# Kernel optimization log

Hardware: AMD Instinct MI355X
Metric: run time of the kernel (lower is better)

Reference implementation:

```python
import jax, jax.numpy as jnp
import numpy as np

B, S, D, H, DI, L = 16, 80, 512, 64, 2048, 6  # batch, seq, d_model, d_lstm(=d_v), d_inner, n_layers
EPS = 1e-6


def _layer_norm(x, g, b):
    m = jnp.mean(x, axis=-1, keepdims=True)
    v = jnp.mean((x - m) ** 2, axis=-1, keepdims=True)
    return (x - m) * jax.lax.rsqrt(v + EPS) * g + b


def _lstm_last(gx, whh):
    # gx: [T, N, 4H] precomputed input-to-gate projections (bias=False LSTM)
    N = gx.shape[1]
    Hh = whh.shape[1]
    init = (jnp.zeros((N, Hh), gx.dtype), jnp.zeros((N, Hh), gx.dtype))

    def step(carry, g_in):
        h, c = carry
        gates = g_in + h @ whh.T  # [N, 4H], torch gate order i,f,g,o
        i, f, g, o = jnp.split(gates, 4, axis=-1)
        c = jax.nn.sigmoid(f) * c + jax.nn.sigmoid(i) * jnp.tanh(g)
        h = jax.nn.sigmoid(o) * jnp.tanh(c)
        return (h, c), None

    (h, _), _ = jax.lax.scan(step, init, gx)
    return h  # [N, H]


def _perm_indices():
    # deterministic janossy permutation: identity with position i swapped to last
    idx = np.arange(S)
    P = np.tile(idx, (S, 1))
    P[idx, idx] = S - 1
    P[idx, S - 1] = idx
    return jnp.asarray(P)  # [S, S]


def _janossy_layer(q, g, b, wih, whh, wfc, P):
    # q: [B, S, D]
    x = _layer_norm(q, g, b)
    # project inputs to gates once, then gather permutations of the projection
    xg = jnp.einsum('bsd,gd->sbg', x, wih)  # [S, B, 4H]
    pg = xg[P]  # [S_i, S_t, B, 4H]: for each output position i, the permuted sequence
    pg = pg.transpose(1, 0, 2, 3).reshape(S, S * B, 4 * H)  # time-major, fold i into batch
    h = _lstm_last(pg, whh)  # [S*B, H]
    h = h.reshape(S, B, H).transpose(1, 0, 2)  # [B, S, H]
    return h @ wfc.T + q  # fc (dropout=identity in eval) + residual


def _ffn(q, g, b, w1, b1, w2, b2):
    x = _layer_norm(q, g, b)
    return jax.nn.relu(x @ w1.T + b1) @ w2.T + b2 + q


def setup_inputs() -> dict:
    key = jax.random.key(0)
    ks = jax.random.split(key, 10)
    n = lambda k, s, sc: jax.random.normal(k, s, jnp.float32) * sc
    return {
        'src_seq': jax.random.normal(ks[0], (B, S, D), jnp.float32),
        'trg_seq': jax.random.normal(ks[1], (B, S, D), jnp.float32),
        'ln1_g': jnp.ones((L, D), jnp.float32),
        'ln1_b': jnp.zeros((L, D), jnp.float32),
        'wih': n(ks[2], (L, 4 * H, D), 0.04),
        'whh': n(ks[3], (L, 4 * H, H), 0.1),
        'wfc': n(ks[4], (L, D, H), 0.05),
        'ln2_g': jnp.ones((L, D), jnp.float32),
        'ln2_b': jnp.zeros((L, D), jnp.float32),
        'w1': n(ks[5], (L, DI, D), 0.03),
        'b1': jnp.zeros((L, DI), jnp.float32),
        'w2': n(ks[6], (L, D, DI), 0.02),
        'b2': jnp.zeros((L, D), jnp.float32),
        'lnf_g': jnp.ones((D,), jnp.float32),
        'lnf_b': jnp.zeros((D,), jnp.float32),
        'wprj': n(ks[7], (1, D), 0.05),
    }


def reference(src_seq, trg_seq, ln1_g, ln1_b, wih, whh, wfc, ln2_g, ln2_b,
              w1, b1, w2, b2, lnf_g, lnf_b, wprj):
    P = _perm_indices()
    x = src_seq
    for l in range(L):  # small fixed layer count
        x = _janossy_layer(x, ln1_g[l], ln1_b[l], wih[l], whh[l], wfc[l], P)
        x = _ffn(x, ln2_g[l], ln2_b[l], w1[l], b1[l], w2[l], b2[l])
    x = _layer_norm(x, lnf_g, lnf_b)
    seq_logit = x @ wprj.T  # [B, S, 1]
    return seq_logit
```

## Files before the change

kernel.cpp:

```cpp
#include <hip/hip_runtime.h>
#include <hip/hip_bf16.h>

#define B_ 16
#define S_ 80
#define D_ 512
#define H_ 64
#define DI_ 2048
#define L_ 6
#define G4H 256
#define NROW (B_ * S_)
#define EPS_ 1e-6f

typedef __attribute__((ext_vector_type(8))) short short8;
typedef __attribute__((ext_vector_type(4))) float f32x4;

__device__ __forceinline__ float sigmoidf_(float x) {
    return __fdividef(1.0f, 1.0f + __expf(-x));
}
__device__ __forceinline__ float tanh_(float x) {
    return __fdividef(2.0f, 1.0f + __expf(-2.0f * x)) - 1.0f;
}
__device__ __forceinline__ short f2bf(float f) {
    __hip_bfloat16 h = __float2bfloat16(f);
    return *reinterpret_cast<short*>(&h);
}

__device__ __forceinline__ void lds_barrier() {
    __asm__ volatile("s_waitcnt lgkmcnt(0)\n\ts_barrier" ::: "memory");
}

__global__ __launch_bounds__(256)
void w2bf_all_kernel(const float* __restrict__ s0, int n0, __hip_bfloat16* __restrict__ d0,
                     const float* __restrict__ s1, int n1, __hip_bfloat16* __restrict__ d1,
                     const float* __restrict__ s2, int n2, __hip_bfloat16* __restrict__ d2,
                     const float* __restrict__ s3, int n3, __hip_bfloat16* __restrict__ d3) {
    int i = blockIdx.x * 256 + threadIdx.x;
    const float* s; __hip_bfloat16* d;
    if (i < n0)      { s = s0; d = d0; }
    else if ((i -= n0) < n1) { s = s1; d = d1; }
    else if ((i -= n1) < n2) { s = s2; d = d2; }
    else if ((i -= n2) < n3) { s = s3; d = d3; }
    else return;
    float4 v = reinterpret_cast<const float4*>(s)[i];
    short4 o;
    o.x = f2bf(v.x); o.y = f2bf(v.y); o.z = f2bf(v.z); o.w = f2bf(v.w);
    reinterpret_cast<short4*>(d)[i] = o;
}

__global__ __launch_bounds__(256)
void ln_kernel(const float* __restrict__ x, const float* __restrict__ g,
               const float* __restrict__ b, __hip_bfloat16* __restrict__ out) {
    int row = blockIdx.x;
    int t = threadIdx.x;
    const float* xr = x + (size_t)row * D_;
    float v0 = xr[t], v1 = xr[t + 256];
    __shared__ float ws4[4], qs4[4];
    float s = v0 + v1;
    #pragma unroll
    for (int o = 32; o > 0; o >>= 1) s += __shfl_down(s, o);
    if ((t & 63) == 0) ws4[t >> 6] = s;
    __syncthreads();
    float m = (ws4[0] + ws4[1] + ws4[2] + ws4[3]) * (1.0f / (float)D_);
    float d0 = v0 - m, d1 = v1 - m;
    float q = d0 * d0 + d1 * d1;
    #pragma unroll
    for (int o = 32; o > 0; o >>= 1) q += __shfl_down(q, o);
    if ((t & 63) == 0) qs4[t >> 6] = q;
    __syncthreads();
    float rs = rsqrtf((qs4[0] + qs4[1] + qs4[2] + qs4[3]) * (1.0f / (float)D_) + EPS_);
    __hip_bfloat16* orow = out + (size_t)row * D_;
    orow[t]       = __float2bfloat16(d0 * rs * g[t]       + b[t]);
    orow[t + 256] = __float2bfloat16(d1 * rs * g[t + 256] + b[t + 256]);
}

template<int WITH_BIAS, int WITH_RELU, int WITH_RES, int OUT_MODE>
__global__ __launch_bounds__(256)
void mfma_gemm(const __hip_bfloat16* __restrict__ A, const __hip_bfloat16* __restrict__ W,
               const float* __restrict__ bias, const float* __restrict__ res,
               void* __restrict__ C, int M, int N, int K) {
    const int LDT = 72;
    __shared__ short As[64 * LDT];
    __shared__ short Ws[64 * LDT];

    int tid  = threadIdx.x;
    int wave = tid >> 6, lane = tid & 63;
    int quad = lane >> 4, l16 = lane & 15;
    int m_off = (wave >> 1) * 32, n_off = (wave & 1) * 32;
    int m0 = blockIdx.y * 64, n0 = blockIdx.x * 64;

    int r = tid >> 2, c = tid & 3;
    const short* Ag = reinterpret_cast<const short*>(A);
    const short* Wg = reinterpret_cast<const short*>(W);

    f32x4 acc00 = {0.f,0.f,0.f,0.f}, acc01 = acc00, acc10 = acc00, acc11 = acc00;

    short8 avA[2], avW[2];
    auto load_tile = [&](int k0) {
        const short* arow = &Ag[(size_t)(m0 + r) * K + k0 + c * 16];
        avA[0] = *reinterpret_cast<const short8*>(arow);
        avA[1] = *reinterpret_cast<const short8*>(arow + 8);
        const short* wrow = &Wg[(size_t)(n0 + r) * K + k0 + c * 16];
        avW[0] = *reinterpret_cast<const short8*>(wrow);
        avW[1] = *reinterpret_cast<const short8*>(wrow + 8);
    };

    load_tile(0);
    for (int k0 = 0; k0 < K; k0 += 64) {
        lds_barrier();
        *reinterpret_cast<short8*>(&As[r * LDT + c * 16])     = avA[0];
        *reinterpret_cast<short8*>(&As[r * LDT + c * 16 + 8]) = avA[1];
        *reinterpret_cast<short8*>(&Ws[r * LDT + c * 16])     = avW[0];
        *reinterpret_cast<short8*>(&Ws[r * LDT + c * 16 + 8]) = avW[1];
        lds_barrier();
        if (k0 + 64 < K) load_tile(k0 + 64);

        #pragma unroll
        for (int kc = 0; kc < 2; kc++) {
            short8 a0 = *reinterpret_cast<const short8*>(&As[(m_off + l16) * LDT + kc * 32 + quad * 8]);
            short8 a1 = *reinterpret_cast<const short8*>(&As[(m_off + 16 + l16) * LDT + kc * 32 + quad * 8]);
            short8 b0 = *reinterpret_cast<const short8*>(&Ws[(n_off + l16) * LDT + kc * 32 + quad * 8]);
            short8 b1 = *reinterpret_cast<const short8*>(&Ws[(n_off + 16 + l16) * LDT + kc * 32 + quad * 8]);
            acc00 = __builtin_amdgcn_mfma_f32_16x16x32_bf16(a0, b0, acc00, 0, 0, 0);
            acc01 = __builtin_amdgcn_mfma_f32_16x16x32_bf16(a0, b1, acc01, 0, 0, 0);
            acc10 = __builtin_amdgcn_mfma_f32_16x16x32_bf16(a1, b0, acc10, 0, 0, 0);
            acc11 = __builtin_amdgcn_mfma_f32_16x16x32_bf16(a1, b1, acc11, 0, 0, 0);
        }
    }

    f32x4 accs[2][2] = {{acc00, acc01}, {acc10, acc11}};
    #pragma unroll
    for (int fi = 0; fi < 2; fi++) {
        #pragma unroll
        for (int fj = 0; fj < 2; fj++) {
            int coln = n0 + n_off + fj * 16 + l16;
            float bv = WITH_BIAS ? bias[coln] : 0.0f;
            #pragma unroll
            for (int rr = 0; rr < 4; rr++) {
                int rowm = m0 + m_off + fi * 16 + quad * 4 + rr;
                float v = accs[fi][fj][rr];
                if (WITH_BIAS) v += bv;
                if (WITH_RELU) v = fmaxf(v, 0.0f);
                if (WITH_RES)  v += res[(size_t)rowm * N + coln];
                if (OUT_MODE == 0) {
                    reinterpret_cast<float*>(C)[(size_t)rowm * N + coln] = v;
                } else if (OUT_MODE == 1) {
                    reinterpret_cast<__hip_bfloat16*>(C)[(size_t)rowm * N + coln] = __float2bfloat16(v);
                } else {
                    int b_ = rowm / S_;
                    int s_ = rowm - b_ * S_;
                    int gate = coln >> 6, u = coln & 63;
                    int half = b_ >> 3, slot = b_ & 7;
                    reinterpret_cast<float*>(C)[
                        ((((size_t)(s_ * 2 + half) * 4 + gate) * 64 + u) << 3) + slot] = v;
                }
            }
        }
    }
}

__global__ __launch_bounds__(256)
void lstm_fc_kernel(const float* __restrict__ xg5,
                    const float* __restrict__ whh,
                    const __hip_bfloat16* __restrict__ wfcb,
                    const float* __restrict__ g2,
                    const float* __restrict__ b2v,
                    float* __restrict__ xcur,
                    __hip_bfloat16* __restrict__ lnb) {
    const int i    = blockIdx.x;
    const int bh   = blockIdx.y;
    const int tid  = threadIdx.x;
    const int wave = tid >> 6, lane = tid & 63;
    const int quad = lane >> 4, l16 = lane & 15;
    const int unit = wave * 16 + l16;

    short8 bfrag[4][2];
    #pragma unroll
    for (int g = 0; g < 4; g++) {
        const float* wr = &whh[(size_t)(g * 64 + unit) * H_];
        #pragma unroll
        for (int kc = 0; kc < 2; kc++) {
            float4 x0 = *(const float4*)(wr + kc * 32 + quad * 8);
            float4 x1 = *(const float4*)(wr + kc * 32 + quad * 8 + 4);
            short8 v;
            v[0] = f2bf(x0.x); v[1] = f2bf(x0.y); v[2] = f2bf(x0.z); v[3] = f2bf(x0.w);
            v[4] = f2bf(x1.x); v[5] = f2bf(x1.y); v[6] = f2bf(x1.z); v[7] = f2bf(x1.w);
            bfrag[g][kc] = v;
        }
    }

    __shared__ __attribute__((aligned(16))) short hsh[2][16][72];
    __shared__ float sred[4][4][2][2];
    for (int idx = tid; idx < 2 * 16 * 72; idx += 256)
        reinterpret_cast<short*>(hsh)[idx] = 0;

    float cst[2] = {0.f, 0.f};

    size_t xoff[4];
    #pragma unroll
    for (int g = 0; g < 4; g++)
        xoff[g] = ((((size_t)bh * 4 + g) * 64 + unit) << 3) + quad * 2;

    auto xload = [&](float2 (&xv)[4], int t) {
        int s = (t == i) ? (S_ - 1) : ((t == S_ - 1) ? i : t);
        const float* base = xg5 + (size_t)s * 4096;
        #pragma unroll
        for (int g = 0; g < 4; g++)
            xv[g] = *reinterpret_cast<const float2*>(base + xoff[g]);
    };

    float2 xvA[4], xvB[4];
    xload(xvA, 0);
    xload(xvB, 1);

    lds_barrier();

    const f32x4 zacc = {0.f, 0.f, 0.f, 0.f};

    auto stepv = [&](int t, float2 (&xc)[4]) {
        const int pb = t & 1;
        short8 af0 = *reinterpret_cast<const short8*>(&hsh[pb][l16][quad * 8]);
        short8 af1 = *reinterpret_cast<const short8*>(&hsh[pb][l16][32 + quad * 8]);

        f32x4 p0 = __builtin_amdgcn_mfma_f32_16x16x32_bf16(af0, bfrag[0][0], zacc, 0, 0, 0);
        f32x4 q0 = __builtin_amdgcn_mfma_f32_16x16x32_bf16(af1, bfrag[0][1], zacc, 0, 0, 0);
        f32x4 p1 = __builtin_amdgcn_mfma_f32_16x16x32_bf16(af0, bfrag[1][0], zacc, 0, 0, 0);
        f32x4 q1 = __builtin_amdgcn_mfma_f32_16x16x32_bf16(af1, bfrag[1][1], zacc, 0, 0, 0);
        f32x4 p2 = __builtin_amdgcn_mfma_f32_16x16x32_bf16(af0, bfrag[2][0], zacc, 0, 0, 0);
        f32x4 q2 = __builtin_amdgcn_mfma_f32_16x16x32_bf16(af1, bfrag[2][1], zacc, 0, 0, 0);
        f32x4 p3 = __builtin_amdgcn_mfma_f32_16x16x32_bf16(af0, bfrag[3][0], zacc, 0, 0, 0);
        f32x4 q3 = __builtin_amdgcn_mfma_f32_16x16x32_bf16(af1, bfrag[3][1], zacc, 0, 0, 0);

        float gi0 = p0[0] + q0[0] + xc[0].x, gi1 = p0[1] + q0[1] + xc[0].y;
        float gf0 = p1[0] + q1[0] + xc[1].x, gf1 = p1[1] + q1[1] + xc[1].y;
        float gg0 = p2[0] + q2[0] + xc[2].x, gg1 = p2[1] + q2[1] + xc[2].y;
        float go0 = p3[0] + q3[0] + xc[3].x, go1 = p3[1] + q3[1] + xc[3].y;

        if (t + 2 < S_) xload(xc, t + 2);

        {
            float ig = sigmoidf_(gi0);
            float fg = sigmoidf_(gf0);
            float gv = tanh_(gg0);
            float og = sigmoidf_(go0);
            float cc = fg * cst[0] + ig * gv;
            cst[0] = cc;
            hsh[pb ^ 1][quad * 4 + 0][unit] = f2bf(og * tanh_(cc));
        }
        {
            float ig = sigmoidf_(gi1);
            float fg = sigmoidf_(gf1);
            float gv = tanh_(gg1);
            float og = sigmoidf_(go1);
            float cc = fg * cst[1] + ig * gv;
            cst[1] = cc;
            hsh[pb ^ 1][quad * 4 + 1][unit] = f2bf(og * tanh_(cc));
        }
        lds_barrier();
    };

    for (int t = 0; t < S_; t += 2) { stepv(t, xvA); stepv(t + 1, xvB); }

    {
        const short* wf = reinterpret_cast<const short*>(wfcb);
        short8 af0 = *reinterpret_cast<const short8*>(&hsh[0][l16][quad * 8]);
        short8 af1 = *reinterpret_cast<const short8*>(&hsh[0][l16][32 + quad * 8]);

        f32x4 facc[8];
        #pragma unroll
        for (int nn = 0; nn < 8; nn++) {
            int col16 = (wave * 8 + nn) * 16 + l16;
            short8 w0 = *reinterpret_cast<const short8*>(&wf[(size_t)col16 * H_ + quad * 8]);
            short8 w1 = *reinterpret_cast<const short8*>(&wf[(size_t)col16 * H_ + 32 + quad * 8]);
            f32x4 a = __builtin_amdgcn_mfma_f32_16x16x32_bf16(af0, w0, zacc, 0, 0, 0);
            facc[nn] = __builtin_amdgcn_mfma_f32_16x16x32_bf16(af1, w1, a, 0, 0, 0);
        }

        float xn[8][2];
        float ssum[2] = {0.f, 0.f}, sq[2] = {0.f, 0.f};
        #pragma unroll
        for (int nn = 0; nn < 8; nn++) {
            int col = (wave * 8 + nn) * 16 + l16;
            #pragma unroll
            for (int rr = 0; rr < 2; rr++) {
                int b = bh * 8 + quad * 2 + rr;
                size_t adr = ((size_t)b * S_ + i) * D_ + col;
                float v = facc[nn][rr] + xcur[adr];
                xn[nn][rr] = v;
                xcur[adr] = v;
                ssum[rr] += v;
                sq[rr]   += v * v;
            }
        }
        #pragma unroll
        for (int m = 1; m < 16; m <<= 1) {
            ssum[0] += __shfl_xor(ssum[0], m); ssum[1] += __shfl_xor(ssum[1], m);
            sq[0]   += __shfl_xor(sq[0], m);   sq[1]   += __shfl_xor(sq[1], m);
        }
        if (l16 == 0) {
            #pragma unroll
            for (int rr = 0; rr < 2; rr++) {
                sred[wave][quad][rr][0] = ssum[rr];
                sred[wave][quad][rr][1] = sq[rr];
            }
        }
        lds_barrier();
        float mmean[2], rstd[2];
        #pragma unroll
        for (int rr = 0; rr < 2; rr++) {
            float s = sred[0][quad][rr][0] + sred[1][quad][rr][0]
                    + sred[2][quad][rr][0] + sred[3][quad][rr][0];
            float q = sred[0][quad][rr][1] + sred[1][quad][rr][1]
                    + sred[2][quad][rr][1] + sred[3][quad][rr][1];
            float m = s * (1.0f / (float)D_);
            mmean[rr] = m;
            rstd[rr]  = rsqrtf(q * (1.0f / (float)D_) - m * m + EPS_);
        }
        #pragma unroll
        for (int nn = 0; nn < 8; nn++) {
            int col = (wave * 8 + nn) * 16 + l16;
            float gv = g2[col], bv = b2v[col];
            #pragma unroll
            for (int rr = 0; rr < 2; rr++) {
                int b = bh * 8 + quad * 2 + rr;
                lnb[((size_t)b * S_ + i) * D_ + col] =
                    __float2bfloat16((xn[nn][rr] - mmean[rr]) * rstd[rr] * gv + bv);
            }
        }
    }
}

__global__ __launch_bounds__(256)
void final_kernel(const float* __restrict__ x, const float* __restrict__ g,
                  const float* __restrict__ b, const float* __restrict__ wprj,
                  float* __restrict__ out) {
    int row = blockIdx.x;
    int t = threadIdx.x;
    const float* xr = x + (size_t)row * D_;
    float v0 = xr[t], v1 = xr[t + 256];
    __shared__ float red[256];
    red[t] = v0 + v1;
    __syncthreads();
    for (int o = 128; o > 0; o >>= 1) { if (t < o) red[t] += red[t + o]; __syncthreads(); }
    float m = red[0] * (1.0f / (float)D_);
    __syncthreads();
    float d0 = v0 - m, d1 = v1 - m;
    red[t] = d0 * d0 + d1 * d1;
    __syncthreads();
    for (int o = 128; o > 0; o >>= 1) { if (t < o) red[t] += red[t + o]; __syncthreads(); }
    float rs = rsqrtf(red[0] * (1.0f / (float)D_) + EPS_);
    __syncthreads();
    float y0 = (d0 * rs * g[t] + b[t]) * wprj[t];
    float y1 = (d1 * rs * g[t + 256] + b[t + 256]) * wprj[t + 256];
    red[t] = y0 + y1;
    __syncthreads();
    for (int o = 128; o > 0; o >>= 1) { if (t < o) red[t] += red[t + o]; __syncthreads(); }
    if (t == 0) out[row] = red[0];
}

extern "C" void kernel_launch(void* const* d_in, const int* in_sizes, int n_in,
                              void* d_out, int out_size, void* d_ws, size_t ws_size,
                              hipStream_t stream) {
    const float* src   = (const float*)d_in[0];
    const float* ln1_g = (const float*)d_in[2];
    const float* ln1_b = (const float*)d_in[3];
    const float* wih   = (const float*)d_in[4];
    const float* whh   = (const float*)d_in[5];
    const float* wfc   = (const float*)d_in[6];
    const float* ln2_g = (const float*)d_in[7];
    const float* ln2_b = (const float*)d_in[8];
    const float* w1    = (const float*)d_in[9];
    const float* b1    = (const float*)d_in[10];
    const float* w2    = (const float*)d_in[11];
    const float* b2    = (const float*)d_in[12];
    const float* lnf_g = (const float*)d_in[13];
    const float* lnf_b = (const float*)d_in[14];
    const float* wprj  = (const float*)d_in[15];
    float* out = (float*)d_out;

    char* ws = (char*)d_ws;
    float* xcur = (float*)ws;                       ws += (size_t)NROW * D_  * 4;
    __hip_bfloat16* lnb = (__hip_bfloat16*)ws;      ws += (size_t)NROW * D_  * 2;
    float* xg5  = (float*)ws;                       ws += (size_t)S_ * 4096  * 4;
    __hip_bfloat16* f1  = (__hip_bfloat16*)ws;      ws += (size_t)NROW * DI_ * 2;
    __hip_bfloat16* wihb = (__hip_bfloat16*)ws;     ws += (size_t)L_ * G4H * D_ * 2;
    __hip_bfloat16* wfcb = (__hip_bfloat16*)ws;     ws += (size_t)L_ * D_ * H_ * 2;
    __hip_bfloat16* w1b  = (__hip_bfloat16*)ws;     ws += (size_t)L_ * DI_ * D_ * 2;
    __hip_bfloat16* w2b  = (__hip_bfloat16*)ws;     ws += (size_t)L_ * D_ * DI_ * 2;

    {
        int n0 = L_ * G4H * D_ / 4;
        int n1 = L_ * D_ * H_ / 4;
        int n2 = L_ * DI_ * D_ / 4;
        int n3 = L_ * D_ * DI_ / 4;
        int total = n0 + n1 + n2 + n3;
        w2bf_all_kernel<<<(total + 255) / 256, 256, 0, stream>>>(
            wih, n0, wihb, wfc, n1, wfcb, w1, n2, w1b, w2, n3, w2b);
    }

    hipMemcpyAsync(xcur, src, (size_t)NROW * D_ * sizeof(float),
                   hipMemcpyDeviceToDevice, stream);

    for (int l = 0; l < L_; l++) {
        ln_kernel<<<NROW, 256, 0, stream>>>(xcur, ln1_g + (size_t)l * D_,
                                            ln1_b + (size_t)l * D_, lnb);
        mfma_gemm<0, 0, 0, 2><<<dim3(G4H / 64, NROW / 64), 256, 0, stream>>>(
            lnb, wihb + (size_t)l * G4H * D_, nullptr, nullptr, xg5, NROW, G4H, D_);
        lstm_fc_kernel<<<dim3(S_, 2), 256, 0, stream>>>(
            xg5, whh + (size_t)l * G4H * H_, wfcb + (size_t)l * D_ * H_,
            ln2_g + (size_t)l * D_, ln2_b + (size_t)l * D_, xcur, lnb);
        mfma_gemm<1, 1, 0, 1><<<dim3(DI_ / 64, NROW / 64), 256, 0, stream>>>(
            lnb, w1b + (size_t)l * DI_ * D_, b1 + (size_t)l * DI_, nullptr, f1, NROW, DI_, D_);
        mfma_gemm<1, 0, 1, 0><<<dim3(D_ / 64, NROW / 64), 256, 0, stream>>>(
            f1, w2b + (size_t)l * D_ * DI_, b2 + (size_t)l * D_, xcur, xcur, NROW, D_, DI_);
    }
    final_kernel<<<NROW, 256, 0, stream>>>(xcur, lnf_g, lnf_b, wprj, out);
}
```

Measured before the change: 692.9 us.

## Fuse layer-norm into input-projection GEMM via row stats from FFN epilogue

Removes the standalone layer-norm kernel before each Janossy layer. The FFN down-projection GEMM now writes per-row partial sums and sums of squares into a small stats buffer, and an initial stats kernel does the same for layer 0. The input-projection GEMM reads fp32 activations, normalizes them on the fly with gamma/beta, and converts to bf16 before staging to LDS. This saves one launch and a bf16 round-trip per layer, but it computes variance as E[x^2]-m^2, which is less numerically stable, and the projection GEMM now loads twice as many A bytes.

Measured after the change: 718.9 us. 1.04x slower.

```diff
diff --git a/kernel.cpp b/kernel.cpp
--- a/kernel.cpp
+++ b/kernel.cpp
@@ -48,34 +48,31 @@
 }
 
 __global__ __launch_bounds__(256)
-void ln_kernel(const float* __restrict__ x, const float* __restrict__ g,
-               const float* __restrict__ b, __hip_bfloat16* __restrict__ out) {
+void stats0_kernel(const float* __restrict__ x, float* __restrict__ stats) {
     int row = blockIdx.x;
     int t = threadIdx.x;
     const float* xr = x + (size_t)row * D_;
     float v0 = xr[t], v1 = xr[t + 256];
+    float s = v0 + v1, q = v0 * v0 + v1 * v1;
     __shared__ float ws4[4], qs4[4];
-    float s = v0 + v1;
     #pragma unroll
-    for (int o = 32; o > 0; o >>= 1) s += __shfl_down(s, o);
-    if ((t & 63) == 0) ws4[t >> 6] = s;
-    __syncthreads();
-    float m = (ws4[0] + ws4[1] + ws4[2] + ws4[3]) * (1.0f / (float)D_);
-    float d0 = v0 - m, d1 = v1 - m;
-    float q = d0 * d0 + d1 * d1;
-    #pragma unroll
-    for (int o = 32; o > 0; o >>= 1) q += __shfl_down(q, o);
-    if ((t & 63) == 0) qs4[t >> 6] = q;
-    __syncthreads();
-    float rs = rsqrtf((qs4[0] + qs4[1] + qs4[2] + qs4[3]) * (1.0f / (float)D_) + EPS_);
-    __hip_bfloat16* orow = out + (size_t)row * D_;
-    orow[t]       = __float2bfloat16(d0 * rs * g[t]       + b[t]);
-    orow[t + 256] = __float2bfloat16(d1 * rs * g[t + 256] + b[t + 256]);
-}
-
-template<int WITH_BIAS, int WITH_RELU, int WITH_RES, int OUT_MODE>
+    for (int o = 32; o > 0; o >>= 1) { s += __shfl_down(s, o); q += __shfl_down(q, o); }
+    if ((t & 63) == 0) { ws4[t >> 6] = s; qs4[t >> 6] = q; }
+    __syncthreads();
+    if (t == 0) {
+        stats[(size_t)row * 16 + 0] = ws4[0] + ws4[1] + ws4[2] + ws4[3];
+        stats[(size_t)row * 16 + 1] = qs4[0] + qs4[1] + qs4[2] + qs4[3];
+    } else if (t < 8) {
+        stats[(size_t)row * 16 + t * 2]     = 0.f;
+        stats[(size_t)row * 16 + t * 2 + 1] = 0.f;
+    }
+}
+
+template<int A_MODE, int WITH_BIAS, int WITH_RELU, int WITH_RES, int OUT_MODE, int WRITE_STATS>
 __global__ __launch_bounds__(256)
-void mfma_gemm(const __hip_bfloat16* __restrict__ A, const __hip_bfloat16* __restrict__ W,
+void mfma_gemm(const void* __restrict__ Ain, const __hip_bfloat16* __restrict__ W,
+               const float* __restrict__ gamma, const float* __restrict__ beta,
+               const float* __restrict__ stats_in, float* __restrict__ stats_out,
                const float* __restrict__ bias, const float* __restrict__ res,
                void* __restrict__ C, int M, int N, int K) {
     const int LDT = 72;
@@ -89,28 +86,74 @@
     int m0 = blockIdx.y * 64, n0 = blockIdx.x * 64;
 
     int r = tid >> 2, c = tid & 3;
-    const short* Ag = reinterpret_cast<const short*>(A);
+    const short* Ag = reinterpret_cast<const short*>(Ain);
+    const float* Af = reinterpret_cast<const float*>(Ain);
     const short* Wg = reinterpret_cast<const short*>(W);
 
+    float mr = 0.f, rsr = 0.f;
+    if constexpr (A_MODE == 1) {
+        const float* sp = stats_in + (size_t)(m0 + r) * 16;
+        float s = 0.f, q = 0.f;
+        #pragma unroll
+        for (int p = 0; p < 4; p++) {
+            float4 v = *reinterpret_cast<const float4*>(sp + p * 4);
+            s += v.x + v.z;  q += v.y + v.w;
+        }
+        mr  = s * (1.0f / 512.0f);
+        rsr = rsqrtf(q * (1.0f / 512.0f) - mr * mr + EPS_);
+    }
+
     f32x4 acc00 = {0.f,0.f,0.f,0.f}, acc01 = acc00, acc10 = acc00, acc11 = acc00;
 
-    short8 avA[2], avW[2];
+    short8 avA[2];
+    float4 avAf[4];
+    short8 avW[2];
     auto load_tile = [&](int k0) {
-        const short* arow = &Ag[(size_t)(m0 + r) * K + k0 + c * 16];
-        avA[0] = *reinterpret_cast<const short8*>(arow);
-        avA[1] = *reinterpret_cast<const short8*>(arow + 8);
+        if constexpr (A_MODE == 1) {
+            const float* arow = Af + (size_t)(m0 + r) * K + k0 + c * 16;
+            avAf[0] = *reinterpret_cast<const float4*>(arow);
+            avAf[1] = *reinterpret_cast<const float4*>(arow + 4);
+            avAf[2] = *reinterpret_cast<const float4*>(arow + 8);
+            avAf[3] = *reinterpret_cast<const float4*>(arow + 12);
+        } else {
+            const short* arow = &Ag[(size_t)(m0 + r) * K + k0 + c * 16];
+            avA[0] = *reinterpret_cast<const short8*>(arow);
+            avA[1] = *reinterpret_cast<const short8*>(arow + 8);
+        }
         const short* wrow = &Wg[(size_t)(n0 + r) * K + k0 + c * 16];
         avW[0] = *reinterpret_cast<const short8*>(wrow);
         avW[1] = *reinterpret_cast<const short8*>(wrow + 8);
     };
 
+    auto store_tile = [&](int k0) {
+        if constexpr (A_MODE == 1) {
+            const float* gp = gamma + k0 + c * 16;
+            const float* bp = beta  + k0 + c * 16;
+            short tmp[16];
+            #pragma unroll
+            for (int j = 0; j < 4; j++) {
+                float4 g4 = *reinterpret_cast<const float4*>(gp + j * 4);
+                float4 b4 = *reinterpret_cast<const float4*>(bp + j * 4);
+                float4 a4 = avAf[j];
+                tmp[j * 4 + 0] = f2bf((a4.x - mr) * rsr * g4.x + b4.x);
+                tmp[j * 4 + 1] = f2bf((a4.y - mr) * rsr * g4.y + b4.y);
+                tmp[j * 4 + 2] = f2bf((a4.z - mr) * rsr * g4.z + b4.z);
+                tmp[j * 4 + 3] = f2bf((a4.w - mr) * rsr * g4.w + b4.w);
+            }
+            *reinterpret_cast<short8*>(&As[r * LDT + c * 16])     = *reinterpret_cast<short8*>(&tmp[0]);
+            *reinterpret_cast<short8*>(&As[r * LDT + c * 16 + 8]) = *reinterpret_cast<short8*>(&tmp[8]);
+        } else {
+            *reinterpret_cast<short8*>(&As[r * LDT + c * 16])     = avA[0];
+            *reinterpret_cast<short8*>(&As[r * LDT + c * 16 + 8]) = avA[1];
+        }
+        *reinterpret_cast<short8*>(&Ws[r * LDT + c * 16])     = avW[0];
+        *reinterpret_cast<short8*>(&Ws[r * LDT + c * 16 + 8]) = avW[1];
+    };
+
     load_tile(0);
     for (int k0 = 0; k0 < K; k0 += 64) {
         lds_barrier();
-        *reinterpret_cast<short8*>(&As[r * LDT + c * 16])     = avA[0];
-        *reinterpret_cast<short8*>(&As[r * LDT + c * 16 + 8]) = avA[1];
-        *reinterpret_cast<short8*>(&Ws[r * LDT + c * 16])     = avW[0];
-        *reinterpret_cast<short8*>(&Ws[r * LDT + c * 16 + 8]) = avW[1];
+        store_tile(k0);
         lds_barrier();
         if (k0 + 64 < K) load_tile(k0 + 64);
 
@@ -127,6 +170,14 @@
         }
     }
 
+    float psum[2][4], psq[2][4];
+    if constexpr (WRITE_STATS) {
+        #pragma unroll
+        for (int fi = 0; fi < 2; fi++)
+            #pragma unroll
+            for (int rr = 0; rr < 4; rr++) { psum[fi][rr] = 0.f; psq[fi][rr] = 0.f; }
+    }
+
     f32x4 accs[2][2] = {{acc00, acc01}, {acc10, acc11}};
     #pragma unroll
     for (int fi = 0; fi < 2; fi++) {
@@ -141,6 +192,7 @@
                 if (WITH_BIAS) v += bv;
                 if (WITH_RELU) v = fmaxf(v, 0.0f);
                 if (WITH_RES)  v += res[(size_t)rowm * N + coln];
+                if constexpr (WRITE_STATS) { psum[fi][rr] += v; psq[fi][rr] += v * v; }
                 if (OUT_MODE == 0) {
                     reinterpret_cast<float*>(C)[(size_t)rowm * N + coln] = v;
                 } else if (OUT_MODE == 1) {
@@ -154,6 +206,29 @@
                         ((((size_t)(s_ * 2 + half) * 4 + gate) * 64 + u) << 3) + slot] = v;
                 }
             }
+        }
+    }
+
+    if constexpr (WRITE_STATS) {
+        __shared__ float sredf[2][64][2];
+        #pragma unroll
+        for (int fi = 0; fi < 2; fi++)
+            #pragma unroll
+            for (int rr = 0; rr < 4; rr++) {
+                float s = psum[fi][rr], q = psq[fi][rr];
+                #pragma unroll
+                for (int m = 1; m < 16; m <<= 1) { s += __shfl_xor(s, m); q += __shfl_xor(q, m); }
+                if (l16 == 0) {
+                    int rowb = m_off + fi * 16 + quad * 4 + rr;
+                    sredf[wave & 1][rowb][0] = s;
+                    sredf[wave & 1][rowb][1] = q;
+                }
+            }
+        lds_barrier();
+        if (tid < 128) {
+            int rowb = tid >> 1, vv = tid & 1;
+            stats_out[(size_t)(m0 + rowb) * 16 + blockIdx.x * 2 + vv] =
+                sredf[0][rowb][vv] + sredf[1][rowb][vv];
         }
     }
 }
@@ -381,6 +456,7 @@
     float* xcur = (float*)ws;                       ws += (size_t)NROW * D_  * 4;
     __hip_bfloat16* lnb = (__hip_bfloat16*)ws;      ws += (size_t)NROW * D_  * 2;
     float* xg5  = (float*)ws;                       ws += (size_t)S_ * 4096  * 4;
+    float* stats = (float*)ws;                      ws += (size_t)NROW * 16 * 4;
     __hip_bfloat16* f1  = (__hip_bfloat16*)ws;      ws += (size_t)NROW * DI_ * 2;
     __hip_bfloat16* wihb = (__hip_bfloat16*)ws;     ws += (size_t)L_ * G4H * D_ * 2;
     __hip_bfloat16* wfcb = (__hip_bfloat16*)ws;     ws += (size_t)L_ * D_ * H_ * 2;
@@ -399,19 +475,22 @@
 
     hipMemcpyAsync(xcur, src, (size_t)NROW * D_ * sizeof(float),
                    hipMemcpyDeviceToDevice, stream);
+    stats0_kernel<<<NROW, 256, 0, stream>>>(xcur, stats);
 
     for (int l = 0; l < L_; l++) {
-        ln_kernel<<<NROW, 256, 0, stream>>>(xcur, ln1_g + (size_t)l * D_,
-                                            ln1_b + (size_t)l * D_, lnb);
-        mfma_gemm<0, 0, 0, 2><<<dim3(G4H / 64, NROW / 64), 256, 0, stream>>>(
-            lnb, wihb + (size_t)l * G4H * D_, nullptr, nullptr, xg5, NROW, G4H, D_);
+        mfma_gemm<1, 0, 0, 0, 2, 0><<<dim3(G4H / 64, NROW / 64), 256, 0, stream>>>(
+            xcur, wihb + (size_t)l * G4H * D_,
+            ln1_g + (size_t)l * D_, ln1_b + (size_t)l * D_, stats, nullptr,
+            nullptr, nullptr, xg5, NROW, G4H, D_);
         lstm_fc_kernel<<<dim3(S_, 2), 256, 0, stream>>>(
             xg5, whh + (size_t)l * G4H * H_, wfcb + (size_t)l * D_ * H_,
             ln2_g + (size_t)l * D_, ln2_b + (size_t)l * D_, xcur, lnb);
-        mfma_gemm<1, 1, 0, 1><<<dim3(DI_ / 64, NROW / 64), 256, 0, stream>>>(
-            lnb, w1b + (size_t)l * DI_ * D_, b1 + (size_t)l * DI_, nullptr, f1, NROW, DI_, D_);
-        mfma_gemm<1, 0, 1, 0><<<dim3(D_ / 64, NROW / 64), 256, 0, stream>>>(
-            f1, w2b + (size_t)l * D_ * DI_, b2 + (size_t)l * D_, xcur, xcur, NROW, D_, DI_);
+        mfma_gemm<0, 1, 1, 0, 1, 0><<<dim3(DI_ / 64, NROW / 64), 256, 0, stream>>>(
+            lnb, w1b + (size_t)l * DI_ * D_, nullptr, nullptr, nullptr, nullptr,
+            b1 + (size_t)l * DI_, nullptr, f1, NROW, DI_, D_);
+        mfma_gemm<0, 1, 0, 1, 0, 1><<<dim3(D_ / 64, NROW / 64), 256, 0, stream>>>(
+            f1, w2b + (size_t)l * D_ * DI_, nullptr, nullptr, nullptr, stats,
+            b2 + (size_t)l * D_, xcur, xcur, NROW, D_, DI_);
     }
     final_kernel<<<NROW, 256, 0, stream>>>(xcur, lnf_g, lnf_b, wprj, out);
 }
```
